# Performance work log

Measured on AMD Instinct MI355X. Metric: run time of the kernel, lower is better.

Reference implementation:

```python
import jax, jax.numpy as jnp
import numpy as np

B, T, D, H, E = 2, 1024, 1024, 4096, 8


def setup_inputs() -> dict:
    key = jax.random.key(0)
    ks = jax.random.split(key, 6)
    x = jax.random.normal(ks[0], (B, T, D), dtype=jnp.float32)
    padding_mask = jnp.zeros((B, T), dtype=bool)
    # Gate: Linear(D, E, bias=False) -> weight (E, D)
    Wg = jax.random.normal(ks[1], (E, D), dtype=jnp.float32) * (1.0 / np.sqrt(D))
    # Stacked expert FFN params (torch Linear layout: weight (out, in))
    W1 = jax.random.normal(ks[2], (E, H, D), dtype=jnp.float32) * (1.0 / np.sqrt(D))
    b1 = jax.random.normal(ks[3], (E, H), dtype=jnp.float32) * 0.01
    W2 = jax.random.normal(ks[4], (E, D, H), dtype=jnp.float32) * (1.0 / np.sqrt(H))
    b2 = jax.random.normal(ks[5], (E, D), dtype=jnp.float32) * 0.01
    return {"x": x, "padding_mask": padding_mask, "Wg": Wg, "W1": W1, "b1": b1, "W2": W2, "b2": b2}


def _top2_gate(xt, pm, Wg):
    # xt: (nt, D) flattened tokens, pm: (nt,) bool padding mask
    nt, ec = xt.shape[0], Wg.shape[0]
    logits = (xt @ Wg.T).astype(jnp.float32)            # use_fp32=True
    gate_value = jax.nn.softmax(logits, axis=-1)        # (nt, E)
    gate_value = jnp.where(pm[:, None], 0.0, gate_value)
    top2_idx = jax.lax.top_k(gate_value, 2)[1]          # (nt, 2)
    keep = jax.nn.one_hot(top2_idx, ec, dtype=bool).any(axis=1)  # (nt, E) True at top1/top2
    gate_weights = jnp.where(keep, gate_value, 0.0)
    s = gate_weights.sum(axis=1, keepdims=True)
    s = jnp.where(s == 0.0, 1.0, s)
    gate_weights = gate_weights / s
    # load-balance loss: fraction of top-1 assignments vs mean gate prob per expert
    nt_real = (~pm).sum().astype(jnp.float32)
    top1_counts = (jax.nn.one_hot(top2_idx[:, 0], ec, dtype=jnp.float32)
                   * (~pm)[:, None].astype(jnp.float32)).sum(axis=0)  # (E,)
    lb_loss = ec * ((top1_counts / nt_real) * (gate_value.sum(axis=0) / nt_real)).sum()
    return lb_loss, gate_weights, gate_value


def reference(x, padding_mask, Wg, W1, b1, W2, b2):
    Bx, Tx, Dx = x.shape
    xt = x.reshape(-1, Dx)                   # (nt, D)
    pm = padding_mask.reshape(-1)            # (nt,)
    lb_loss, gw, gate_value = _top2_gate(xt, pm, Wg)
    gw = gw.astype(x.dtype)                  # (nt, E)
    # Expert FFNs (dense over experts; routing weights are zero except top-2)
    h = jax.nn.relu(jnp.einsum('nd,ehd->neh', xt, W1) + b1)   # (nt, E, H)
    y = jnp.einsum('neh,edh->ned', h, W2) + b2                # (nt, E, D)
    out = jnp.einsum('ne,ned->nd', gw, y).reshape(Bx, Tx, Dx)
    return out, gate_value, lb_loss
```

## Files before the change

kernel.cpp:

```cpp
#include <hip/hip_runtime.h>
#include <hip/hip_bf16.h>
#include <stdint.h>


#define NTOK 2048
#define DDIM 1024
#define HDIM 4096
#define NEXP 8
#define KSPLIT 2

typedef float  f32x4  __attribute__((ext_vector_type(4)));
typedef __bf16 bf16x8 __attribute__((ext_vector_type(8)));
typedef __bf16 bf16x4 __attribute__((ext_vector_type(4)));

typedef const __attribute__((address_space(1))) void g1_t;
typedef __attribute__((address_space(3))) void l3_t;
__device__ __forceinline__ void gld16(const void* g, void* l) {
  __builtin_amdgcn_global_load_lds((g1_t*)g, (l3_t*)l, 16, 0, 0);
}

__global__ void init_kernel(int* fill) {
  int t = threadIdx.x;
  if (t < NEXP) fill[t] = 0;
}

__global__ __launch_bounds__(256)
void conv_kernel(const float* __restrict__ src, __bf16* __restrict__ dst, long n8) {
  long i = (long)blockIdx.x * 256 + threadIdx.x;
  long stride = (long)gridDim.x * 256;
  for (; i < n8; i += stride) {
    f32x4 a = ((const f32x4*)src)[2 * i];
    f32x4 b = ((const f32x4*)src)[2 * i + 1];
    bf16x8 o;
#pragma unroll
    for (int q = 0; q < 4; ++q) { o[q] = (__bf16)a[q]; o[q + 4] = (__bf16)b[q]; }
    ((bf16x8*)dst)[i] = o;
  }
}

__global__ __launch_bounds__(256)
void zero_y_kernel(float* __restrict__ y) {
  size_t i = (size_t)blockIdx.x * 256 + threadIdx.x;
  ((f32x4*)y)[i] = (f32x4){0.f, 0.f, 0.f, 0.f};
}

__global__ __launch_bounds__(256)
void gate_kernel(const float* __restrict__ x, const unsigned char* __restrict__ pmask,
                 const float* __restrict__ Wg, float* __restrict__ gate_out,
                 int* __restrict__ tix, float* __restrict__ twt,
                 __bf16* __restrict__ xbf)
{
  int wave = threadIdx.x >> 6, lane = threadIdx.x & 63;
  int t = blockIdx.x * 4 + wave;
  const f32x4* x4 = (const f32x4*)(x + (size_t)t * DDIM);
  const f32x4* w4 = (const f32x4*)Wg;
  bf16x4* xb4 = (bf16x4*)(xbf + (size_t)t * DDIM);
  float acc[NEXP];
#pragma unroll
  for (int e = 0; e < NEXP; ++e) acc[e] = 0.f;
#pragma unroll
  for (int i = 0; i < 4; ++i) {
    f32x4 xv = x4[i * 64 + lane];
    bf16x4 xo;
#pragma unroll
    for (int q = 0; q < 4; ++q) xo[q] = (__bf16)xv[q];
    xb4[i * 64 + lane] = xo;
#pragma unroll
    for (int e = 0; e < NEXP; ++e) {
      f32x4 wv = w4[e * 256 + i * 64 + lane];
      acc[e] += xv[0]*wv[0] + xv[1]*wv[1] + xv[2]*wv[2] + xv[3]*wv[3];
    }
  }
#pragma unroll
  for (int e = 0; e < NEXP; ++e) {
    float v = acc[e];
#pragma unroll
    for (int off = 32; off > 0; off >>= 1) v += __shfl_xor(v, off, 64);
    acc[e] = v;
  }
  if (lane == 0) {
    bool pm = pmask[t] != 0;
    float m = acc[0];
#pragma unroll
    for (int e = 1; e < NEXP; ++e) m = fmaxf(m, acc[e]);
    float g[NEXP]; float s = 0.f;
#pragma unroll
    for (int e = 0; e < NEXP; ++e) { g[e] = expf(acc[e] - m); s += g[e]; }
    float inv = 1.f / s;
#pragma unroll
    for (int e = 0; e < NEXP; ++e) g[e] *= inv;
    if (pm) {
#pragma unroll
      for (int e = 0; e < NEXP; ++e) g[e] = 0.f;
    }
    int i1 = 0;
#pragma unroll
    for (int e = 1; e < NEXP; ++e) if (g[e] > g[i1]) i1 = e;
    int i2 = -1;
#pragma unroll
    for (int e = 0; e < NEXP; ++e) if (e != i1 && (i2 < 0 || g[e] > g[i2])) i2 = e;
    float w1 = g[i1], w2 = g[i2], ss = w1 + w2;
    if (ss == 0.f) ss = 1.f;
    w1 /= ss; w2 /= ss;
#pragma unroll
    for (int e = 0; e < NEXP; ++e) gate_out[(size_t)t * NEXP + e] = g[e];
    tix[2*t] = i1; tix[2*t+1] = i2;
    twt[2*t] = w1; twt[2*t+1] = w2;
  }
}

__global__ __launch_bounds__(1024)
void stats_kernel(const float* __restrict__ gate_out, const int* __restrict__ tix,
                  const unsigned char* __restrict__ pmask,
                  int* __restrict__ ecount, int* __restrict__ offs,
                  float* __restrict__ lb_out)
{
  int tid = threadIdx.x, lane = tid & 63, wv = tid >> 6;
  float lg[NEXP]; float lt1[NEXP]; int lec[NEXP]; float ln = 0.f;
#pragma unroll
  for (int e = 0; e < NEXP; ++e) { lg[e] = 0.f; lt1[e] = 0.f; lec[e] = 0; }
#pragma unroll
  for (int it = 0; it < NTOK / 1024; ++it) {
    int t = tid + it * 1024;
    f32x4 g0 = ((const f32x4*)(gate_out + (size_t)t * NEXP))[0];
    f32x4 g1 = ((const f32x4*)(gate_out + (size_t)t * NEXP))[1];
    lg[0] += g0[0]; lg[1] += g0[1]; lg[2] += g0[2]; lg[3] += g0[3];
    lg[4] += g1[0]; lg[5] += g1[1]; lg[6] += g1[2]; lg[7] += g1[3];
    if (!pmask[t]) {
      int i1 = tix[2*t], i2 = tix[2*t+1];
      lt1[i1] += 1.f; lec[i1] += 1; lec[i2] += 1; ln += 1.f;
    }
  }
#pragma unroll
  for (int e = 0; e < NEXP; ++e) {
#pragma unroll
    for (int off = 32; off > 0; off >>= 1) {
      lg[e]  += __shfl_xor(lg[e],  off, 64);
      lt1[e] += __shfl_xor(lt1[e], off, 64);
      lec[e] += __shfl_xor(lec[e], off, 64);
    }
  }
#pragma unroll
  for (int off = 32; off > 0; off >>= 1) ln += __shfl_xor(ln, off, 64);
  __shared__ float sg[16][NEXP], st[16][NEXP], sn[16];
  __shared__ int   se[16][NEXP];
  if (lane == 0) {
#pragma unroll
    for (int e = 0; e < NEXP; ++e) { sg[wv][e] = lg[e]; st[wv][e] = lt1[e]; se[wv][e] = lec[e]; }
    sn[wv] = ln;
  }
  __syncthreads();
  if (tid == 0) {
    float G[NEXP] = {0}, T1[NEXP] = {0}; int EC[NEXP] = {0}; float N = 0.f;
    for (int w = 0; w < 16; ++w) {
      N += sn[w];
#pragma unroll
      for (int e = 0; e < NEXP; ++e) { G[e] += sg[w][e]; T1[e] += st[w][e]; EC[e] += se[w][e]; }
    }
    int o = 0;
    for (int e = 0; e < NEXP; ++e) { ecount[e] = EC[e]; offs[e] = o; o += EC[e]; }
    if (N <= 0.f) N = 1.f;
    float lb = 0.f;
    for (int e = 0; e < NEXP; ++e) lb += (T1[e] / N) * (G[e] / N);
    lb_out[0] = (float)NEXP * lb;
  }
}

__global__ __launch_bounds__(256)
void compact_kernel(const unsigned char* __restrict__ pmask, const int* __restrict__ tix,
                    const int* __restrict__ offs, int* __restrict__ fill,
                    int* __restrict__ tok_list, int* __restrict__ slot_of)
{
  int t = blockIdx.x * 256 + threadIdx.x;
  int lane = threadIdx.x & 63;
  bool pm = pmask[t] != 0;
#pragma unroll
  for (int j = 0; j < 2; ++j) {
    int e = pm ? -1 : tix[2*t + j];
    int pos = -1;
#pragma unroll
    for (int ex = 0; ex < NEXP; ++ex) {
      unsigned long long mask = __ballot(e == ex);
      if (mask) {
        int leader = (int)(__ffsll((long long)mask) - 1);
        int base = 0;
        if (lane == leader) base = atomicAdd(&fill[ex], (int)__popcll(mask));
        base = __shfl(base, leader, 64);
        if (e == ex)
          pos = offs[ex] + base + (int)__popcll(mask & ((1ull << lane) - 1ull));
      }
    }
    if (e >= 0) { tok_list[pos] = t; slot_of[2*t + j] = pos; }
    else slot_of[2*t + j] = -1;
  }
}


__global__ __launch_bounds__(256)
void gemm1_kernel(const __bf16* __restrict__ xbf, const __bf16* __restrict__ w1bf,
                  const float* __restrict__ b1, const int* __restrict__ ecount,
                  const int* __restrict__ offs, const int* __restrict__ tok_list,
                  __bf16* __restrict__ hbuf)
{
  const int NTILE = HDIM / 128;
  const int MTILE = NTOK / 128;
  int bid = blockIdx.x;
  int e = bid / (MTILE * NTILE);
  int rem = bid % (MTILE * NTILE);
  int mt = rem / NTILE, nt = rem % NTILE;
  int cnt = ecount[e];
  if (mt * 128 >= cnt) return;
  int off = offs[e];

  __shared__ __bf16 As[3][128 * 32];
  __shared__ __bf16 Bs[3][128 * 32];

  int tid = threadIdx.x, lane = tid & 63, wave = tid >> 6;
  int wm = wave >> 1, wn = wave & 1;

  const __bf16* aP[2];
  const __bf16* bP[2];
#pragma unroll
  for (int c = 0; c < 2; ++c) {
    int row = c * 64 + (tid >> 2);
    int cd = (tid & 3) ^ ((row >> 1) & 3);
    int mrow = mt * 128 + row;
    int tok = tok_list[off + ((mrow < cnt) ? mrow : 0)];
    aP[c] = xbf + (size_t)tok * DDIM + cd * 8;
    bP[c] = w1bf + (size_t)e * HDIM * DDIM + (size_t)(nt * 128 + row) * DDIM + cd * 8;
  }
  int cg = ((lane >> 4) ^ ((lane >> 1) & 3)) << 3;

  f32x4 acc[4][4];
#pragma unroll
  for (int m = 0; m < 4; ++m)
#pragma unroll
    for (int n = 0; n < 4; ++n) acc[m][n] = (f32x4){0.f, 0.f, 0.f, 0.f};

  const int NIT = DDIM / 32;
#pragma unroll
  for (int pt = 0; pt < 2; ++pt)
#pragma unroll
    for (int c = 0; c < 2; ++c) {
      gld16(aP[c] + pt * 32, &As[pt][(c * 64 + wave * 16) * 32]);
      gld16(bP[c] + pt * 32, &Bs[pt][(c * 64 + wave * 16) * 32]);
    }

  for (int it = 0; it < NIT; ++it) {
    int cur = it % 3;
    if (it + 1 < NIT) asm volatile("s_waitcnt vmcnt(4)" ::: "memory");
    else              asm volatile("s_waitcnt vmcnt(0)" ::: "memory");
    __builtin_amdgcn_s_barrier();
    __builtin_amdgcn_sched_barrier(0);
    if (it + 2 < NIT) {
      int nb = (it + 2) % 3;
      int k0 = (it + 2) * 32;
#pragma unroll
      for (int c = 0; c < 2; ++c) {
        gld16(aP[c] + k0, &As[nb][(c * 64 + wave * 16) * 32]);
        gld16(bP[c] + k0, &Bs[nb][(c * 64 + wave * 16) * 32]);
      }
    }
    bf16x8 af[4], bfr[4];
#pragma unroll
    for (int m = 0; m < 4; ++m) af[m]  = *(const bf16x8*)&As[cur][(wm*64 + m*16 + (lane & 15)) * 32 + cg];
#pragma unroll
    for (int n = 0; n < 4; ++n) bfr[n] = *(const bf16x8*)&Bs[cur][(wn*64 + n*16 + (lane & 15)) * 32 + cg];
#pragma unroll
    for (int m = 0; m < 4; ++m)
#pragma unroll
      for (int n = 0; n < 4; ++n)
        acc[m][n] = __builtin_amdgcn_mfma_f32_16x16x32_bf16(af[m], bfr[n], acc[m][n], 0, 0, 0);
  }

#pragma unroll
  for (int n = 0; n < 4; ++n) {
    int col = nt * 128 + wn * 64 + n * 16 + (lane & 15);
    float bias = b1[e * HDIM + col];
#pragma unroll
    for (int m = 0; m < 4; ++m) {
#pragma unroll
      for (int j = 0; j < 4; ++j) {
        int mr = mt * 128 + wm * 64 + m * 16 + ((lane >> 4) << 2) + j;
        if (mr < cnt) {
          float v = fmaxf(acc[m][n][j] + bias, 0.f);
          hbuf[(size_t)(off + mr) * HDIM + col] = (__bf16)v;
        }
      }
    }
  }
}

__global__ __launch_bounds__(256)
void gemm2_kernel(const __bf16* __restrict__ hbuf, const __bf16* __restrict__ w2bf,
                  const int* __restrict__ ecount, const int* __restrict__ offs,
                  float* __restrict__ ybuf)
{
  const int NTILE = DDIM / 128;
  const int MTILE = NTOK / 128;
  int bid = blockIdx.x;
  int e = bid / (MTILE * NTILE * KSPLIT);
  int rem = bid % (MTILE * NTILE * KSPLIT);
  int mt = rem / (NTILE * KSPLIT);
  int rem2 = rem % (NTILE * KSPLIT);
  int nt = rem2 / KSPLIT, kc = rem2 % KSPLIT;
  int cnt = ecount[e];
  if (mt * 128 >= cnt) return;
  int off = offs[e];

  __shared__ __bf16 As[3][128 * 32];
  __shared__ __bf16 Bs[3][128 * 32];

  int tid = threadIdx.x, lane = tid & 63, wave = tid >> 6;
  int wm = wave >> 1, wn = wave & 1;

  const __bf16* aP[2];
  const __bf16* bP[2];
#pragma unroll
  for (int c = 0; c < 2; ++c) {
    int row = c * 64 + (tid >> 2);
    int cd = (tid & 3) ^ ((row >> 1) & 3);
    aP[c] = hbuf + (size_t)(off + mt * 128 + row) * HDIM + cd * 8;
    bP[c] = w2bf + (size_t)e * DDIM * HDIM + (size_t)(nt * 128 + row) * HDIM + cd * 8;
  }
  int cg = ((lane >> 4) ^ ((lane >> 1) & 3)) << 3;

  f32x4 acc[4][4];
#pragma unroll
  for (int m = 0; m < 4; ++m)
#pragma unroll
    for (int n = 0; n < 4; ++n) acc[m][n] = (f32x4){0.f, 0.f, 0.f, 0.f};

  const int KCH = HDIM / KSPLIT;
  const int NIT = KCH / 32;
  int kbeg = kc * KCH;
#pragma unroll
  for (int pt = 0; pt < 2; ++pt)
#pragma unroll
    for (int c = 0; c < 2; ++c) {
      gld16(aP[c] + kbeg + pt * 32, &As[pt][(c * 64 + wave * 16) * 32]);
      gld16(bP[c] + kbeg + pt * 32, &Bs[pt][(c * 64 + wave * 16) * 32]);
    }

  for (int it = 0; it < NIT; ++it) {
    int cur = it % 3;
    if (it + 1 < NIT) asm volatile("s_waitcnt vmcnt(4)" ::: "memory");
    else              asm volatile("s_waitcnt vmcnt(0)" ::: "memory");
    __builtin_amdgcn_s_barrier();
    __builtin_amdgcn_sched_barrier(0);
    if (it + 2 < NIT) {
      int nb = (it + 2) % 3;
      int k0 = kbeg + (it + 2) * 32;
#pragma unroll
      for (int c = 0; c < 2; ++c) {
        gld16(aP[c] + k0, &As[nb][(c * 64 + wave * 16) * 32]);
        gld16(bP[c] + k0, &Bs[nb][(c * 64 + wave * 16) * 32]);
      }
    }
    bf16x8 af[4], bfr[4];
#pragma unroll
    for (int m = 0; m < 4; ++m) af[m]  = *(const bf16x8*)&As[cur][(wm*64 + m*16 + (lane & 15)) * 32 + cg];
#pragma unroll
    for (int n = 0; n < 4; ++n) bfr[n] = *(const bf16x8*)&Bs[cur][(wn*64 + n*16 + (lane & 15)) * 32 + cg];
#pragma unroll
    for (int m = 0; m < 4; ++m)
#pragma unroll
      for (int n = 0; n < 4; ++n)
        acc[m][n] = __builtin_amdgcn_mfma_f32_16x16x32_bf16(af[m], bfr[n], acc[m][n], 0, 0, 0);
  }

#pragma unroll
  for (int m = 0; m < 4; ++m) {
#pragma unroll
    for (int j = 0; j < 4; ++j) {
      int mr = mt * 128 + wm * 64 + m * 16 + ((lane >> 4) << 2) + j;
      if (mr >= cnt) continue;
      int slot = off + mr;
#pragma unroll
      for (int n = 0; n < 4; ++n) {
        int col = nt * 128 + wn * 64 + n * 16 + (lane & 15);
        atomicAdd(&ybuf[(size_t)slot * DDIM + col], acc[m][n][j]);
      }
    }
  }
}

__global__ __launch_bounds__(256)
void combine_kernel(const float* __restrict__ ybuf, const int* __restrict__ slot_of,
                    const int* __restrict__ tix, const float* __restrict__ twt,
                    const float* __restrict__ b2, float* __restrict__ out)
{
  int t = blockIdx.x;
  int d4 = threadIdx.x;
  int sA = slot_of[2*t], sB = slot_of[2*t + 1];
  f32x4 r = (f32x4){0.f, 0.f, 0.f, 0.f};
  if (sA >= 0) {
    float wA = twt[2*t];
    f32x4 y = ((const f32x4*)(ybuf + (size_t)sA * DDIM))[d4];
    f32x4 b = ((const f32x4*)(b2 + (size_t)tix[2*t] * DDIM))[d4];
    r += wA * (y + b);
  }
  if (sB >= 0) {
    float wB = twt[2*t + 1];
    f32x4 y = ((const f32x4*)(ybuf + (size_t)sB * DDIM))[d4];
    f32x4 b = ((const f32x4*)(b2 + (size_t)tix[2*t + 1] * DDIM))[d4];
    r += wB * (y + b);
  }
  ((f32x4*)(out + (size_t)t * DDIM))[d4] = r;
}

extern "C" void kernel_launch(void* const* d_in, const int* in_sizes, int n_in,
                              void* d_out, int out_size, void* d_ws, size_t ws_size,
                              hipStream_t stream)
{
  const float* x  = (const float*)d_in[0];
  const unsigned char* pm = (const unsigned char*)d_in[1];
  const float* Wg = (const float*)d_in[2];
  const float* W1 = (const float*)d_in[3];
  const float* b1 = (const float*)d_in[4];
  const float* W2 = (const float*)d_in[5];
  const float* b2 = (const float*)d_in[6];
  float* out = (float*)d_out;
  float* gate_out = out + (size_t)NTOK * DDIM;
  float* lb_out = gate_out + (size_t)NTOK * NEXP;

  char* w = (char*)d_ws;
  int*   ecount   = (int*)(w + 0);
  int*   offs     = (int*)(w + 64);
  int*   fill     = (int*)(w + 128);
  int*   tix      = (int*)(w + 512);
  float* twt      = (float*)(w + 512 + 16384);
  int*   tok_list = (int*)(w + 512 + 32768);
  int*   slot_of  = (int*)(w + 512 + 49152);
  uintptr_t p = ((uintptr_t)(w + 512 + 65536) + 255) & ~(uintptr_t)255;
  __bf16* xbf  = (__bf16*)p;
  p += (size_t)NTOK * DDIM * 2;
  __bf16* wbf  = (__bf16*)p;
  p += (size_t)NEXP * HDIM * DDIM * 2;
  __bf16* hbuf = (__bf16*)p;
  p += (size_t)(2 * NTOK + 128) * HDIM * 2;
  float*  ybuf = (float*)p;

  init_kernel<<<1, 64, 0, stream>>>(fill);
  conv_kernel<<<2048, 256, 0, stream>>>(W1, wbf, (long)NEXP * HDIM * DDIM / 8);
  zero_y_kernel<<<(2 * NTOK * DDIM / 4) / 256, 256, 0, stream>>>(ybuf);
  gate_kernel<<<NTOK / 4, 256, 0, stream>>>(x, pm, Wg, gate_out, tix, twt, xbf);
  stats_kernel<<<1, 1024, 0, stream>>>(gate_out, tix, pm, ecount, offs, lb_out);
  compact_kernel<<<NTOK / 256, 256, 0, stream>>>(pm, tix, offs, fill, tok_list, slot_of);
  gemm1_kernel<<<NEXP * (NTOK / 128) * (HDIM / 128), 256, 0, stream>>>(xbf, wbf, b1, ecount, offs, tok_list, hbuf);
  conv_kernel<<<2048, 256, 0, stream>>>(W2, wbf, (long)NEXP * DDIM * HDIM / 8);
  gemm2_kernel<<<NEXP * (NTOK / 128) * (DDIM / 128) * KSPLIT, 256, 0, stream>>>(hbuf, wbf, ecount, offs, ybuf);
  combine_kernel<<<NTOK, 256, 0, stream>>>(ybuf, slot_of, tix, twt, b2, out);
}
```

Before: 258.8 us.

## Fuse prep kernels, overlap W2 conversion with GEMM1, scatter GEMM2 into output

Measured after the change: 286.9 us. 1.11x slower.

```diff
diff --git a/kernel.cpp b/kernel.cpp
--- a/kernel.cpp
+++ b/kernel.cpp
@@ -8,6 +8,9 @@
 #define HDIM 4096
 #define NEXP 8
 #define KSPLIT 2
+#define CONVB 1024
+#define GATEB (NTOK / 4)
+#define ZEROB 512
 
 typedef float  f32x4  __attribute__((ext_vector_type(4)));
 typedef __bf16 bf16x8 __attribute__((ext_vector_type(8)));
@@ -24,10 +27,10 @@
   if (t < NEXP) fill[t] = 0;
 }
 
-__global__ __launch_bounds__(256)
-void conv_kernel(const float* __restrict__ src, __bf16* __restrict__ dst, long n8) {
-  long i = (long)blockIdx.x * 256 + threadIdx.x;
-  long stride = (long)gridDim.x * 256;
+__device__ __forceinline__ void conv_body(int bid, const float* __restrict__ src,
+                                          __bf16* __restrict__ dst, long n8) {
+  long i = (long)bid * 256 + threadIdx.x;
+  long stride = (long)CONVB * 256;
   for (; i < n8; i += stride) {
     f32x4 a = ((const f32x4*)src)[2 * i];
     f32x4 b = ((const f32x4*)src)[2 * i + 1];
@@ -38,20 +41,20 @@
   }
 }
 
-__global__ __launch_bounds__(256)
-void zero_y_kernel(float* __restrict__ y) {
-  size_t i = (size_t)blockIdx.x * 256 + threadIdx.x;
-  ((f32x4*)y)[i] = (f32x4){0.f, 0.f, 0.f, 0.f};
-}
-
-__global__ __launch_bounds__(256)
-void gate_kernel(const float* __restrict__ x, const unsigned char* __restrict__ pmask,
-                 const float* __restrict__ Wg, float* __restrict__ gate_out,
-                 int* __restrict__ tix, float* __restrict__ twt,
-                 __bf16* __restrict__ xbf)
-{
+__device__ __forceinline__ void zero_body(int bid, float* __restrict__ y, long n4) {
+  long i = (long)bid * 256 + threadIdx.x;
+  long stride = (long)ZEROB * 256;
+  for (; i < n4; i += stride) ((f32x4*)y)[i] = (f32x4){0.f, 0.f, 0.f, 0.f};
+}
+
+__device__ __forceinline__ void gate_body(int bid, const float* __restrict__ x,
+                                          const unsigned char* __restrict__ pmask,
+                                          const float* __restrict__ Wg,
+                                          float* __restrict__ gate_out,
+                                          int* __restrict__ tix, float* __restrict__ twt,
+                                          __bf16* __restrict__ xbf) {
   int wave = threadIdx.x >> 6, lane = threadIdx.x & 63;
-  int t = blockIdx.x * 4 + wave;
+  int t = bid * 4 + wave;
   const f32x4* x4 = (const f32x4*)(x + (size_t)t * DDIM);
   const f32x4* w4 = (const f32x4*)Wg;
   bf16x4* xb4 = (bf16x4*)(xbf + (size_t)t * DDIM);
@@ -107,6 +110,21 @@
     tix[2*t] = i1; tix[2*t+1] = i2;
     twt[2*t] = w1; twt[2*t+1] = w2;
   }
+}
+
+__global__ __launch_bounds__(256)
+void preA_kernel(const float* __restrict__ x, const unsigned char* __restrict__ pmask,
+                 const float* __restrict__ Wg, float* __restrict__ gate_out,
+                 int* __restrict__ tix, float* __restrict__ twt,
+                 __bf16* __restrict__ xbf, const float* __restrict__ W1,
+                 __bf16* __restrict__ w1bf, float* __restrict__ out)
+{
+  int bid = blockIdx.x;
+  if (bid < CONVB) { conv_body(bid, W1, w1bf, (long)NEXP * HDIM * DDIM / 8); return; }
+  bid -= CONVB;
+  if (bid < GATEB) { gate_body(bid, x, pmask, Wg, gate_out, tix, twt, xbf); return; }
+  bid -= GATEB;
+  zero_body(bid, out, (long)NTOK * DDIM / 4);
 }
 
 __global__ __launch_bounds__(1024)
@@ -168,8 +186,9 @@
 
 __global__ __launch_bounds__(256)
 void compact_kernel(const unsigned char* __restrict__ pmask, const int* __restrict__ tix,
-                    const int* __restrict__ offs, int* __restrict__ fill,
-                    int* __restrict__ tok_list, int* __restrict__ slot_of)
+                    const float* __restrict__ twt, const int* __restrict__ offs,
+                    int* __restrict__ fill, int* __restrict__ tok_list,
+                    float* __restrict__ wgt_list)
 {
   int t = blockIdx.x * 256 + threadIdx.x;
   int lane = threadIdx.x & 63;
@@ -190,21 +209,21 @@
           pos = offs[ex] + base + (int)__popcll(mask & ((1ull << lane) - 1ull));
       }
     }
-    if (e >= 0) { tok_list[pos] = t; slot_of[2*t + j] = pos; }
-    else slot_of[2*t + j] = -1;
-  }
-}
-
-
-__global__ __launch_bounds__(256)
-void gemm1_kernel(const __bf16* __restrict__ xbf, const __bf16* __restrict__ w1bf,
-                  const float* __restrict__ b1, const int* __restrict__ ecount,
-                  const int* __restrict__ offs, const int* __restrict__ tok_list,
-                  __bf16* __restrict__ hbuf)
+    if (e >= 0) { tok_list[pos] = t; wgt_list[pos] = twt[2*t + j]; }
+  }
+}
+
+
+__device__ __forceinline__ void gemm1_body(int bid, const __bf16* __restrict__ xbf,
+                                           const __bf16* __restrict__ w1bf,
+                                           const float* __restrict__ b1,
+                                           const int* __restrict__ ecount,
+                                           const int* __restrict__ offs,
+                                           const int* __restrict__ tok_list,
+                                           __bf16* __restrict__ hbuf)
 {
   const int NTILE = HDIM / 128;
   const int MTILE = NTOK / 128;
-  int bid = blockIdx.x;
   int e = bid / (MTILE * NTILE);
   int rem = bid % (MTILE * NTILE);
   int mt = rem / NTILE, nt = rem % NTILE;
@@ -292,9 +311,36 @@
 }
 
 __global__ __launch_bounds__(256)
+void gemm1u_kernel(const __bf16* __restrict__ xbf, const __bf16* __restrict__ w1bf,
+                   const float* __restrict__ b1, const int* __restrict__ ecount,
+                   const int* __restrict__ offs, const int* __restrict__ tok_list,
+                   __bf16* __restrict__ hbuf, const float* __restrict__ W2,
+                   __bf16* __restrict__ w2bf)
+{
+  if (blockIdx.x < CONVB) { conv_body(blockIdx.x, W2, w2bf, (long)NEXP * DDIM * HDIM / 8); return; }
+  gemm1_body(blockIdx.x - CONVB, xbf, w1bf, b1, ecount, offs, tok_list, hbuf);
+}
+
+__global__ __launch_bounds__(256)
+void gemm1_kernel(const __bf16* __restrict__ xbf, const __bf16* __restrict__ w1bf,
+                  const float* __restrict__ b1, const int* __restrict__ ecount,
+                  const int* __restrict__ offs, const int* __restrict__ tok_list,
+                  __bf16* __restrict__ hbuf)
+{
+  gemm1_body(blockIdx.x, xbf, w1bf, b1, ecount, offs, tok_list, hbuf);
+}
+
+__global__ __launch_bounds__(256)
+void conv_kernel(const float* __restrict__ src, __bf16* __restrict__ dst, long n8)
+{
+  conv_body(blockIdx.x, src, dst, n8);
+}
+
+__global__ __launch_bounds__(256)
 void gemm2_kernel(const __bf16* __restrict__ hbuf, const __bf16* __restrict__ w2bf,
-                  const int* __restrict__ ecount, const int* __restrict__ offs,
-                  float* __restrict__ ybuf)
+                  const float* __restrict__ b2, const int* __restrict__ ecount,
+                  const int* __restrict__ offs, const int* __restrict__ tok_list,
+                  const float* __restrict__ wgt_list, float* __restrict__ out)
 {
   const int NTILE = DDIM / 128;
   const int MTILE = NTOK / 128;
@@ -369,6 +415,12 @@
         acc[m][n] = __builtin_amdgcn_mfma_f32_16x16x32_bf16(af[m], bfr[n], acc[m][n], 0, 0, 0);
   }
 
+  float b2v[4];
+#pragma unroll
+  for (int n = 0; n < 4; ++n) {
+    int col = nt * 128 + wn * 64 + n * 16 + (lane & 15);
+    b2v[n] = (kc == 0) ? b2[e * DDIM + col] : 0.f;
+  }
 #pragma unroll
   for (int m = 0; m < 4; ++m) {
 #pragma unroll
@@ -376,37 +428,16 @@
       int mr = mt * 128 + wm * 64 + m * 16 + ((lane >> 4) << 2) + j;
       if (mr >= cnt) continue;
       int slot = off + mr;
+      int tok = tok_list[slot];
+      float w = wgt_list[slot];
+      float* obase = out + (size_t)tok * DDIM;
 #pragma unroll
       for (int n = 0; n < 4; ++n) {
         int col = nt * 128 + wn * 64 + n * 16 + (lane & 15);
-        atomicAdd(&ybuf[(size_t)slot * DDIM + col], acc[m][n][j]);
+        atomicAdd(obase + col, w * (acc[m][n][j] + b2v[n]));
       }
     }
   }
-}
-
-__global__ __launch_bounds__(256)
-void combine_kernel(const float* __restrict__ ybuf, const int* __restrict__ slot_of,
-                    const int* __restrict__ tix, const float* __restrict__ twt,
-                    const float* __restrict__ b2, float* __restrict__ out)
-{
-  int t = blockIdx.x;
-  int d4 = threadIdx.x;
-  int sA = slot_of[2*t], sB = slot_of[2*t + 1];
-  f32x4 r = (f32x4){0.f, 0.f, 0.f, 0.f};
-  if (sA >= 0) {
-    float wA = twt[2*t];
-    f32x4 y = ((const f32x4*)(ybuf + (size_t)sA * DDIM))[d4];
-    f32x4 b = ((const f32x4*)(b2 + (size_t)tix[2*t] * DDIM))[d4];
-    r += wA * (y + b);
-  }
-  if (sB >= 0) {
-    float wB = twt[2*t + 1];
-    f32x4 y = ((const f32x4*)(ybuf + (size_t)sB * DDIM))[d4];
-    f32x4 b = ((const f32x4*)(b2 + (size_t)tix[2*t + 1] * DDIM))[d4];
-    r += wB * (y + b);
-  }
-  ((f32x4*)(out + (size_t)t * DDIM))[d4] = r;
 }
 
 extern "C" void kernel_launch(void* const* d_in, const int* in_sizes, int n_in,
@@ -431,24 +462,31 @@
   int*   tix      = (int*)(w + 512);
   float* twt      = (float*)(w + 512 + 16384);
   int*   tok_list = (int*)(w + 512 + 32768);
-  int*   slot_of  = (int*)(w + 512 + 49152);
+  float* wgt_list = (float*)(w + 512 + 49152);
   uintptr_t p = ((uintptr_t)(w + 512 + 65536) + 255) & ~(uintptr_t)255;
   __bf16* xbf  = (__bf16*)p;
   p += (size_t)NTOK * DDIM * 2;
-  __bf16* wbf  = (__bf16*)p;
+  __bf16* w1bf = (__bf16*)p;
   p += (size_t)NEXP * HDIM * DDIM * 2;
   __bf16* hbuf = (__bf16*)p;
   p += (size_t)(2 * NTOK + 128) * HDIM * 2;
-  float*  ybuf = (float*)p;
+  __bf16* w2bf_sep = (__bf16*)p;
+  size_t need = (size_t)((char*)(w2bf_sep + (size_t)NEXP * DDIM * HDIM) - w);
+  bool overlap = (ws_size >= need);
+  __bf16* w2bf = overlap ? w2bf_sep : w1bf;
 
   init_kernel<<<1, 64, 0, stream>>>(fill);
-  conv_kernel<<<2048, 256, 0, stream>>>(W1, wbf, (long)NEXP * HDIM * DDIM / 8);
-  zero_y_kernel<<<(2 * NTOK * DDIM / 4) / 256, 256, 0, stream>>>(ybuf);
-  gate_kernel<<<NTOK / 4, 256, 0, stream>>>(x, pm, Wg, gate_out, tix, twt, xbf);
+  preA_kernel<<<CONVB + GATEB + ZEROB, 256, 0, stream>>>(x, pm, Wg, gate_out, tix, twt, xbf, W1, w1bf, out);
   stats_kernel<<<1, 1024, 0, stream>>>(gate_out, tix, pm, ecount, offs, lb_out);
-  compact_kernel<<<NTOK / 256, 256, 0, stream>>>(pm, tix, offs, fill, tok_list, slot_of);
-  gemm1_kernel<<<NEXP * (NTOK / 128) * (HDIM / 128), 256, 0, stream>>>(xbf, wbf, b1, ecount, offs, tok_list, hbuf);
-  conv_kernel<<<2048, 256, 0, stream>>>(W2, wbf, (long)NEXP * DDIM * HDIM / 8);
-  gemm2_kernel<<<NEXP * (NTOK / 128) * (DDIM / 128) * KSPLIT, 256, 0, stream>>>(hbuf, wbf, ecount, offs, ybuf);
-  combine_kernel<<<NTOK, 256, 0, stream>>>(ybuf, slot_of, tix, twt, b2, out);
-}
+  compact_kernel<<<NTOK / 256, 256, 0, stream>>>(pm, tix, twt, offs, fill, tok_list, wgt_list);
+  if (overlap) {
+    gemm1u_kernel<<<CONVB + NEXP * (NTOK / 128) * (HDIM / 128), 256, 0, stream>>>(
+        xbf, w1bf, b1, ecount, offs, tok_list, hbuf, W2, w2bf);
+  } else {
+    gemm1_kernel<<<NEXP * (NTOK / 128) * (HDIM / 128), 256, 0, stream>>>(
+        xbf, w1bf, b1, ecount, offs, tok_list, hbuf);
+    conv_kernel<<<CONVB, 256, 0, stream>>>(W2, w2bf, (long)NEXP * DDIM * HDIM / 8);
+  }
+  gemm2_kernel<<<NEXP * (NTOK / 128) * (DDIM / 128) * KSPLIT, 256, 0, stream>>>(
+      hbuf, w2bf, b2, ecount, offs, tok_list, wgt_list, out);
+}
```
